# Kernel optimization log

Measured on AMD Instinct MI355X. Metric: run time of the kernel, lower is better.

Reference implementation:

```python
import jax, jax.numpy as jnp
import numpy as np

N_HEADS = 8
TOPK = 32


def setup_inputs() -> dict:
    key = jax.random.key(0)
    ks = jax.random.split(key, 6)
    N, L, Hd = 2, 2048, 512
    s = 1.0 / np.sqrt(Hd).astype(np.float32)
    return {
        "queries": jax.random.normal(ks[0], (N, L, Hd), jnp.float32),
        "keys": jax.random.normal(ks[1], (N, L, Hd), jnp.float32),
        "values": jax.random.normal(ks[2], (N, L, Hd), jnp.float32),
        "Wq": jax.random.normal(ks[3], (Hd, Hd), jnp.float32) * s,
        "bq": jnp.zeros((Hd,), jnp.float32),
        "Wk": jax.random.normal(ks[4], (Hd, Hd), jnp.float32) * s,
        "bk": jnp.zeros((Hd,), jnp.float32),
        "Wv": jax.random.normal(ks[5], (Hd, Hd), jnp.float32) * s,
        "bv": jnp.zeros((Hd,), jnp.float32),
    }


def reference(queries, keys, values, Wq, bq, Wk, bk, Wv, bv):
    N, L, Hd = queries.shape
    S = keys.shape[1]
    H = N_HEADS
    E = Hd // H
    q = (queries @ Wq.T + bq).reshape(N, L, H, E)
    k = (keys @ Wk.T + bk).reshape(N, S, H, E)
    v = (values @ Wv.T + bv).reshape(N, S, H, E)
    temp = 1.0 / np.sqrt(E).astype(np.float32)
    QK = jnp.einsum("nlhe,nshe->nhls", q, k)  # [N,H,L,S]
    topk = min(TOPK, S)
    _, idx = jax.lax.top_k(QK, topk)  # idx: [N,H,L,topk]
    ni = jnp.arange(N)[:, None, None, None]
    hi = jnp.arange(H)[None, :, None, None]
    li = jnp.arange(L)[None, None, :, None]
    keep = jnp.zeros(QK.shape, bool).at[ni, hi, li, idx].set(True)
    # torch: softmax(temp * (QK + mask)) with mask 0 on top-k, -inf elsewhere
    scores = jnp.where(keep, temp * QK, -jnp.inf)
    A = jax.nn.softmax(scores, axis=-1)  # dropout is identity in eval mode
    V = jnp.einsum("nhls,nshd->nlhd", A, v).reshape(N, L, Hd)
    return V, A
```

## Files before the change

kernel.cpp:

```cpp
#include <hip/hip_runtime.h>
#include <cstdint>
#include <cstddef>
#include <math.h>

#define NH     8
#define EH     64
#define HD     512
#define NBATCH 2
#define LSEQ   2048
#define TK     32


using f32x4  = __attribute__((ext_vector_type(4))) float;
using bf16x8 = __attribute__((ext_vector_type(8))) short;

__device__ __forceinline__ unsigned short f2b(float f) {
    unsigned u = __float_as_uint(f);
    return (unsigned short)((u + 0x7FFFu + ((u >> 16) & 1u)) >> 16);
}
__device__ __forceinline__ unsigned f2key(float f) {
    unsigned u = __float_as_uint(f);
    return (u & 0x80000000u) ? ~u : (u | 0x80000000u);
}
__device__ __forceinline__ float key2f(unsigned k) {
    return __uint_as_float((k & 0x80000000u) ? (k ^ 0x80000000u) : ~k);
}

__global__ __launch_bounds__(256) void proj_kernel(
    const float* __restrict__ Xq, const float* __restrict__ Xk, const float* __restrict__ Xv,
    const float* __restrict__ Wq, const float* __restrict__ Bq,
    const float* __restrict__ Wk, const float* __restrict__ Bk,
    const float* __restrict__ Wv, const float* __restrict__ Bv,
    float* __restrict__ ws)
{
    const int z = blockIdx.z;
    const float* X = (z == 0) ? Xq : (z == 1) ? Xk : Xv;
    const float* W = (z == 0) ? Wq : (z == 1) ? Wk : Wv;
    const float* B = (z == 0) ? Bq : (z == 1) ? Bk : Bv;
    float* out = ws + (size_t)z * 2097152;
    unsigned short* khi = (unsigned short*)(ws + 6291456);

    __shared__ float4 Xs[64 * 8];
    __shared__ float4 Ws[64 * 8];

    const int tid = threadIdx.x;
    const int tx = tid & 15, ty = tid >> 4;
    const int m0 = blockIdx.x * 64, n0 = blockIdx.y * 64;

    float acc[4][4];
    #pragma unroll
    for (int i = 0; i < 4; ++i)
        #pragma unroll
        for (int j = 0; j < 4; ++j) acc[i][j] = 0.f;

    for (int k0 = 0; k0 < HD; k0 += 32) {
        #pragma unroll
        for (int it = 0; it < 2; ++it) {
            int f = tid + it * 256;
            int row = f >> 3, c = f & 7;
            int cs = c ^ ((row >> 2) & 7);
            Xs[row * 8 + cs] = *(const float4*)&X[(size_t)(m0 + row) * HD + k0 + c * 4];
            Ws[row * 8 + cs] = *(const float4*)&W[(size_t)(n0 + row) * HD + k0 + c * 4];
        }
        __syncthreads();
        #pragma unroll
        for (int c = 0; c < 8; ++c) {
            float4 av[4], bv4[4];
            #pragma unroll
            for (int i = 0; i < 4; ++i) { int r = ty * 4 + i; av[i]  = Xs[r * 8 + (c ^ ((r >> 2) & 7))]; }
            #pragma unroll
            for (int j = 0; j < 4; ++j) { int r = tx * 4 + j; bv4[j] = Ws[r * 8 + (c ^ ((r >> 2) & 7))]; }
            #pragma unroll
            for (int i = 0; i < 4; ++i)
                #pragma unroll
                for (int j = 0; j < 4; ++j) {
                    acc[i][j] = fmaf(av[i].x, bv4[j].x, acc[i][j]);
                    acc[i][j] = fmaf(av[i].y, bv4[j].y, acc[i][j]);
                    acc[i][j] = fmaf(av[i].z, bv4[j].z, acc[i][j]);
                    acc[i][j] = fmaf(av[i].w, bv4[j].w, acc[i][j]);
                }
        }
        __syncthreads();
    }

    #pragma unroll
    for (int j = 0; j < 4; ++j) {
        int o = n0 + tx * 4 + j;
        float bb = B[o];
        int h = o >> 6, e = o & 63;
        #pragma unroll
        for (int i = 0; i < 4; ++i) {
            int m = m0 + ty * 4 + i;
            int n = m >> 11, s = m & 2047;
            float val = acc[i][j] + bb;
            int head = n * NH + h;
            out[(size_t)head * 131072 + (size_t)s * EH + e] = val;
            if (z == 1) {
                int kt = s >> 4, ks = e >> 5;
                int lane = (((e & 31) >> 3) << 4) | (s & 15);
                size_t idx = ((((size_t)head * 128 + kt) * 2 + ks) * 64 + lane) * 8 + (e & 7);
                khi[idx] = f2b(val);
            }
        }
    }
}

__device__ __forceinline__ unsigned long long sort64_desc(unsigned long long v, int lane) {
    #pragma unroll
    for (int k = 2; k <= 64; k <<= 1)
        #pragma unroll
        for (int j = k >> 1; j >= 1; j >>= 1) {
            unsigned long long o = __shfl_xor(v, j, 64);
            bool up = ((lane & k) != 0);
            bool keepmin = (((lane & j) == 0) == up);
            unsigned long long lo = v < o ? v : o;
            unsigned long long hi = v > o ? v : o;
            v = keepmin ? lo : hi;
        }
    return v;
}
__device__ __forceinline__ unsigned long long merge_top64(unsigned long long a, unsigned long long b, int lane) {
    unsigned long long br = __shfl(b, 63 - lane, 64);
    unsigned long long m = a > br ? a : br;
    #pragma unroll
    for (int j = 32; j >= 1; j >>= 1) {
        unsigned long long o = __shfl_xor(m, j, 64);
        bool keepmax = ((lane & j) == 0);
        unsigned long long mx = m > o ? m : o;
        unsigned long long mn = m < o ? m : o;
        m = keepmax ? mx : mn;
    }
    return m;
}

__global__ __launch_bounds__(512, 4) void attn_kernel(
    const float* __restrict__ ws, float* __restrict__ outV, float* __restrict__ outA)
{
    const float* qw = ws;
    const float* kw = ws + 2097152;
    const float* vw = ws + 4194304;
    const unsigned short* khi = (const unsigned short*)(ws + 6291456);

    __shared__ unsigned short scores16[16 * 2048];
    __shared__ float qs[EH * 16];
    __shared__ unsigned short candArr[8 * 256];
    __shared__ unsigned cnts[8];

    const int tid  = threadIdx.x;
    const int lane = tid & 63;
    const int wv   = tid >> 6;

    unsigned bid = blockIdx.x;
    unsigned id  = (bid & 7u) * 256u + (bid >> 3);
    const int head = (int)(id >> 7);
    const int l0   = (int)(id & 127u) * 16;
    const size_t headoff = (size_t)head * 131072;

    #pragma unroll
    for (int it = 0; it < 2; ++it) {
        int i = tid + it * 512;
        int row = i & 15, e = i >> 4;
        qs[i] = qw[headoff + (size_t)(l0 + row) * EH + e];
    }
    __syncthreads();

    {
        bf16x8 afrag[2];
        #pragma unroll
        for (int ks = 0; ks < 2; ++ks)
            #pragma unroll
            for (int j = 0; j < 8; ++j) {
                int e = ks * 32 + ((lane >> 4) << 3) + j;
                afrag[ks][j] = (short)f2b(qs[e * 16 + (lane & 15)]);
            }

        f32x4 acc[16];
        #pragma unroll
        for (int kt = 0; kt < 16; ++kt) acc[kt] = (f32x4)(0.f);

        const unsigned short* kb = khi + headoff * 2;
        #pragma unroll
        for (int kt = 0; kt < 16; ++kt) {
            int ktg = wv * 16 + kt;
            #pragma unroll
            for (int ks = 0; ks < 2; ++ks) {
                bf16x8 b = *(const bf16x8*)(khi + (size_t)head * 131072 +
                              ((((size_t)ktg * 2 + ks) * 64 + lane) << 3));
                acc[kt] = __builtin_amdgcn_mfma_f32_16x16x32_bf16(afrag[ks], b, acc[kt], 0, 0, 0);
            }
        }
        (void)kb;
        #pragma unroll
        for (int kt = 0; kt < 16; ++kt) {
            int key = wv * 256 + kt * 16 + (lane & 15);
            #pragma unroll
            for (int reg = 0; reg < 4; ++reg) {
                int rr = ((lane >> 4) << 2) + reg;
                scores16[rr * 2048 + key] = (unsigned short)(f2key(acc[kt][reg]) >> 16);
            }
        }
    }
    __syncthreads();

    unsigned short* cand = candArr + wv * 256;
    int   rowS[2][1]; float rowW[2][1];
    int selS[2]; float selW[2];

    #pragma unroll
    for (int rr2 = 0; rr2 < 2; ++rr2) {
        const int r = 2 * wv + rr2;
        const unsigned* srow32 = (const unsigned*)(scores16 + r * 2048);

        unsigned mx = 0;
        #pragma unroll
        for (int t = 0; t < 16; ++t) {
            unsigned vv = srow32[t * 64 + lane];
            unsigned a = vv & 0xFFFFu, b = vv >> 16;
            unsigned ab = a > b ? a : b;
            mx = mx > ab ? mx : ab;
        }
        {
            unsigned v = mx;
            #pragma unroll
            for (int k = 2; k <= 64; k <<= 1)
                #pragma unroll
                for (int j = k >> 1; j >= 1; j >>= 1) {
                    unsigned o = __shfl_xor(v, j);
                    bool up = ((lane & k) == 0);
                    bool keepmin = (((lane & j) == 0) == up);
                    unsigned lo = v < o ? v : o, hi = v > o ? v : o;
                    v = keepmin ? lo : hi;
                }
            mx = __shfl(v, 32);
        }
        const unsigned tau16 = mx;
        const float tauf = key2f(tau16 << 16);
        const unsigned thr16 = f2key(tauf - 0.35f) >> 16;

        if (lane == 0) cnts[wv] = 0;
        #pragma unroll
        for (int t = 0; t < 16; ++t) {
            unsigned vv = srow32[t * 64 + lane];
            unsigned i0 = (unsigned)((t * 64 + lane) * 2);
            if ((vv & 0xFFFFu) >= thr16) {
                unsigned p = atomicAdd(&cnts[wv], 1u);
                if (p < 256) cand[p] = (unsigned short)i0;
            }
            if ((vv >> 16) >= thr16) {
                unsigned p = atomicAdd(&cnts[wv], 1u);
                if (p < 256) cand[p] = (unsigned short)(i0 + 1);
            }
        }
        int Nc = (int)cnts[wv];
        if (Nc > 256) Nc = 256;
        const int nch = (Nc + 63) >> 6;

        unsigned long long best = 0ull;
        for (int c = 0; c < nch; ++c) {
            int p = c * 64 + lane;
            bool valid = p < Nc;
            int si = valid ? (int)cand[p] : 0;
            float sc = 0.f;
            if (valid) {
                const float* krow = kw + headoff + (size_t)si * EH;
                #pragma unroll
                for (int c4 = 0; c4 < 16; ++c4) {
                    float4 kv = *(const float4*)&krow[c4 * 4];
                    sc = fmaf(qs[(c4 * 4 + 0) * 16 + r], kv.x, sc);
                    sc = fmaf(qs[(c4 * 4 + 1) * 16 + r], kv.y, sc);
                    sc = fmaf(qs[(c4 * 4 + 2) * 16 + r], kv.z, sc);
                    sc = fmaf(qs[(c4 * 4 + 3) * 16 + r], kv.w, sc);
                }
            }
            unsigned long long comp = valid
                ? ((((unsigned long long)f2key(sc)) << 32) | (unsigned)(~si))
                : 0ull;
            comp = sort64_desc(comp, lane);
            best = (c == 0) ? comp : merge_top64(best, comp, lane);
        }

        unsigned key32 = (unsigned)(best >> 32);
        int si = (int)(~((unsigned)best)) & 2047;
        float sc = key2f(key32);
        float M = __shfl(sc, 0);
        float ee = (lane < TK) ? __expf(0.125f * (sc - M)) : 0.f;
        float Z = ee;
        #pragma unroll
        for (int d = 1; d < 64; d <<= 1) Z += __shfl_xor(Z, d);
        selS[rr2] = si;
        selW[rr2] = ee / Z;
    }
    rowS[0][0] = selS[0]; rowW[0][0] = selW[0];
    rowS[1][0] = selS[1]; rowW[1][0] = selW[1];

    float* abuf = (float*)((char*)scores16 + wv * 8192);
    const int n = head >> 3, h = head & 7;
    #pragma unroll
    for (int rr2 = 0; rr2 < 2; ++rr2) {
        const int lrow = l0 + 2 * wv + rr2;
        float4* ab4 = (float4*)abuf;
        const float4 z4 = make_float4(0.f, 0.f, 0.f, 0.f);
        #pragma unroll
        for (int u = 0; u < 8; ++u) ab4[u * 64 + lane] = z4;
        if (lane < TK) abuf[rowS[rr2][0]] = rowW[rr2][0];
        float* Arow = outA + ((size_t)head * 2048 + lrow) * 2048;
        #pragma unroll
        for (int u = 0; u < 8; ++u)
            *(float4*)&Arow[(u * 64 + lane) * 4] = ab4[u * 64 + lane];

        float acc = 0.f;
        #pragma unroll
        for (int i = 0; i < TK; ++i) {
            int s_i   = __shfl(rowS[rr2][0], i);
            float w_i = __shfl(rowW[rr2][0], i);
            acc = fmaf(w_i, vw[headoff + (size_t)s_i * EH + lane], acc);
        }
        outV[((size_t)(n * 2048 + lrow)) * 512 + h * 64 + lane] = acc;
    }
}

extern "C" void kernel_launch(void* const* d_in, const int* in_sizes, int n_in,
                              void* d_out, int out_size, void* d_ws, size_t ws_size,
                              hipStream_t stream)
{
    (void)in_sizes; (void)n_in; (void)out_size; (void)ws_size;
    const float* q  = (const float*)d_in[0];
    const float* k  = (const float*)d_in[1];
    const float* v  = (const float*)d_in[2];
    const float* Wq = (const float*)d_in[3];
    const float* bq = (const float*)d_in[4];
    const float* Wk = (const float*)d_in[5];
    const float* bk = (const float*)d_in[6];
    const float* Wv = (const float*)d_in[7];
    const float* bv = (const float*)d_in[8];
    float* ws   = (float*)d_ws;
    float* outV = (float*)d_out;
    float* outA = outV + (size_t)NBATCH * LSEQ * HD;

    proj_kernel<<<dim3(64, 8, 3), 256, 0, stream>>>(q, k, v, Wq, bq, Wk, bk, Wv, bv, ws);
    attn_kernel<<<dim3(2048, 1, 1), 512, 0, stream>>>(ws, outV, outA);
}
```

Before: 246.2 us.

## Coalesce bf16 key staging and replace atomics/shuffles with ballots and readlanes

The projection kernel now stages bf16 keys in shared memory and writes the MFMA-ready layout with 16-byte vector stores instead of scattered 2-byte stores. In the attention kernel, the LDS atomic candidate compaction becomes ballot/popcount prefix compaction. Row scores are held in registers instead of re-read from LDS, and q rows are loaded into registers for exact rescoring. Per-tile MFMA accumulators are shortened in lifetime, and shuffles in the V gather become readlane. These changes raise register use and add LDS usage in the projection kernel.

```diff
diff --git a/kernel.cpp b/kernel.cpp
--- a/kernel.cpp
+++ b/kernel.cpp
@@ -13,6 +13,7 @@
 
 using f32x4  = __attribute__((ext_vector_type(4))) float;
 using bf16x8 = __attribute__((ext_vector_type(8))) short;
+using u16x8  = __attribute__((ext_vector_type(8))) unsigned short;
 
 __device__ __forceinline__ unsigned short f2b(float f) {
     unsigned u = __float_as_uint(f);
@@ -25,6 +26,7 @@
 __device__ __forceinline__ float key2f(unsigned k) {
     return __uint_as_float((k & 0x80000000u) ? (k ^ 0x80000000u) : ~k);
 }
+__device__ __forceinline__ unsigned umax2(unsigned a, unsigned b) { return a > b ? a : b; }
 
 __global__ __launch_bounds__(256) void proj_kernel(
     const float* __restrict__ Xq, const float* __restrict__ Xk, const float* __restrict__ Xv,
@@ -42,6 +44,7 @@
 
     __shared__ float4 Xs[64 * 8];
     __shared__ float4 Ws[64 * 8];
+    __shared__ unsigned short kst[64 * 72];
 
     const int tid = threadIdx.x;
     const int tx = tid & 15, ty = tid >> 4;
@@ -95,12 +98,25 @@
             float val = acc[i][j] + bb;
             int head = n * NH + h;
             out[(size_t)head * 131072 + (size_t)s * EH + e] = val;
-            if (z == 1) {
-                int kt = s >> 4, ks = e >> 5;
-                int lane = (((e & 31) >> 3) << 4) | (s & 15);
-                size_t idx = ((((size_t)head * 128 + kt) * 2 + ks) * 64 + lane) * 8 + (e & 7);
-                khi[idx] = f2b(val);
-            }
+            if (z == 1) kst[(ty * 4 + i) * 72 + e] = f2b(val);
+        }
+    }
+
+    if (z == 1) {
+        __syncthreads();
+        const int head = (m0 >> 11) * NH + (n0 >> 6);
+        const int kt0  = (m0 & 2047) >> 4;
+        #pragma unroll
+        for (int it = 0; it < 2; ++it) {
+            int g = tid + it * 256;
+            int lane_g = g & 63;
+            int rest = g >> 6;
+            int kt = rest >> 1, ksb = rest & 1;
+            int s_loc = kt * 16 + (lane_g & 15);
+            int e0 = ksb * 32 + ((lane_g >> 4) << 3);
+            u16x8 vv = *(const u16x8*)&kst[s_loc * 72 + e0];
+            size_t idx = ((((size_t)head * 128 + (kt0 + kt)) * 2 + ksb) * 64 + lane_g) * 8;
+            *(u16x8*)&khi[idx] = vv;
         }
     }
 }
@@ -144,11 +160,10 @@
     __shared__ unsigned short scores16[16 * 2048];
     __shared__ float qs[EH * 16];
     __shared__ unsigned short candArr[8 * 256];
-    __shared__ unsigned cnts[8];
 
     const int tid  = threadIdx.x;
     const int lane = tid & 63;
-    const int wv   = tid >> 6;
+    const int uwv  = __builtin_amdgcn_readfirstlane(tid) >> 6;
 
     unsigned bid = blockIdx.x;
     unsigned id  = (bid & 7u) * 256u + (bid >> 3);
@@ -174,50 +189,44 @@
                 afrag[ks][j] = (short)f2b(qs[e * 16 + (lane & 15)]);
             }
 
-        f32x4 acc[16];
-        #pragma unroll
-        for (int kt = 0; kt < 16; ++kt) acc[kt] = (f32x4)(0.f);
-
-        const unsigned short* kb = khi + headoff * 2;
         #pragma unroll
         for (int kt = 0; kt < 16; ++kt) {
-            int ktg = wv * 16 + kt;
+            f32x4 acc = (f32x4)(0.f);
+            int ktg = uwv * 16 + kt;
             #pragma unroll
             for (int ks = 0; ks < 2; ++ks) {
                 bf16x8 b = *(const bf16x8*)(khi + (size_t)head * 131072 +
                               ((((size_t)ktg * 2 + ks) * 64 + lane) << 3));
-                acc[kt] = __builtin_amdgcn_mfma_f32_16x16x32_bf16(afrag[ks], b, acc[kt], 0, 0, 0);
-            }
-        }
-        (void)kb;
-        #pragma unroll
-        for (int kt = 0; kt < 16; ++kt) {
-            int key = wv * 256 + kt * 16 + (lane & 15);
-            #pragma unroll
-            for (int reg = 0; reg < 4; ++reg) {
-                int rr = ((lane >> 4) << 2) + reg;
-                scores16[rr * 2048 + key] = (unsigned short)(f2key(acc[kt][reg]) >> 16);
-            }
+                acc = __builtin_amdgcn_mfma_f32_16x16x32_bf16(afrag[ks], b, acc, 0, 0, 0);
+            }
+            int key = uwv * 256 + kt * 16 + (lane & 15);
+            int rbase = (lane >> 4) << 2;
+            #pragma unroll
+            for (int reg = 0; reg < 4; ++reg)
+                scores16[(rbase + reg) * 2048 + key] = (unsigned short)(f2key(acc[reg]) >> 16);
         }
     }
     __syncthreads();
 
-    unsigned short* cand = candArr + wv * 256;
-    int   rowS[2][1]; float rowW[2][1];
+    unsigned short* cand = candArr + uwv * 256;
+    const unsigned long long lmlt = (1ull << lane) - 1ull;
     int selS[2]; float selW[2];
 
     #pragma unroll
     for (int rr2 = 0; rr2 < 2; ++rr2) {
-        const int r = 2 * wv + rr2;
+        const int r = 2 * uwv + rr2;
+        const int lrow = l0 + r;
         const unsigned* srow32 = (const unsigned*)(scores16 + r * 2048);
 
+        unsigned pk[16];
+        #pragma unroll
+        for (int t = 0; t < 16; ++t) pk[t] = srow32[t * 64 + lane];
+
         unsigned mx = 0;
         #pragma unroll
         for (int t = 0; t < 16; ++t) {
-            unsigned vv = srow32[t * 64 + lane];
-            unsigned a = vv & 0xFFFFu, b = vv >> 16;
-            unsigned ab = a > b ? a : b;
-            mx = mx > ab ? mx : ab;
+            unsigned a = pk[t] & 0xFFFFu, b = pk[t] >> 16;
+            mx = umax2(mx, umax2(a, b));
         }
         {
             unsigned v = mx;
@@ -237,40 +246,48 @@
         const float tauf = key2f(tau16 << 16);
         const unsigned thr16 = f2key(tauf - 0.35f) >> 16;
 
-        if (lane == 0) cnts[wv] = 0;
+        int Nc = 0;
         #pragma unroll
         for (int t = 0; t < 16; ++t) {
-            unsigned vv = srow32[t * 64 + lane];
+            unsigned vv = pk[t];
             unsigned i0 = (unsigned)((t * 64 + lane) * 2);
-            if ((vv & 0xFFFFu) >= thr16) {
-                unsigned p = atomicAdd(&cnts[wv], 1u);
+            bool c0 = (vv & 0xFFFFu) >= thr16;
+            bool c1 = (vv >> 16) >= thr16;
+            unsigned long long b0 = __ballot(c0);
+            if (c0) {
+                int p = Nc + __popcll(b0 & lmlt);
                 if (p < 256) cand[p] = (unsigned short)i0;
             }
-            if ((vv >> 16) >= thr16) {
-                unsigned p = atomicAdd(&cnts[wv], 1u);
+            Nc += __popcll(b0);
+            unsigned long long b1 = __ballot(c1);
+            if (c1) {
+                int p = Nc + __popcll(b1 & lmlt);
                 if (p < 256) cand[p] = (unsigned short)(i0 + 1);
             }
-        }
-        int Nc = (int)cnts[wv];
+            Nc += __popcll(b1);
+        }
         if (Nc > 256) Nc = 256;
         const int nch = (Nc + 63) >> 6;
+
+        const float* qrow = qw + headoff + (size_t)lrow * EH;
+        float4 qv[16];
+        #pragma unroll
+        for (int c4 = 0; c4 < 16; ++c4) qv[c4] = *(const float4*)&qrow[c4 * 4];
 
         unsigned long long best = 0ull;
         for (int c = 0; c < nch; ++c) {
             int p = c * 64 + lane;
             bool valid = p < Nc;
             int si = valid ? (int)cand[p] : 0;
+            const float* krow = kw + headoff + (size_t)si * EH;
             float sc = 0.f;
-            if (valid) {
-                const float* krow = kw + headoff + (size_t)si * EH;
-                #pragma unroll
-                for (int c4 = 0; c4 < 16; ++c4) {
-                    float4 kv = *(const float4*)&krow[c4 * 4];
-                    sc = fmaf(qs[(c4 * 4 + 0) * 16 + r], kv.x, sc);
-                    sc = fmaf(qs[(c4 * 4 + 1) * 16 + r], kv.y, sc);
-                    sc = fmaf(qs[(c4 * 4 + 2) * 16 + r], kv.z, sc);
-                    sc = fmaf(qs[(c4 * 4 + 3) * 16 + r], kv.w, sc);
-                }
+            #pragma unroll
+            for (int c4 = 0; c4 < 16; ++c4) {
+                float4 kv = *(const float4*)&krow[c4 * 4];
+                sc = fmaf(qv[c4].x, kv.x, sc);
+                sc = fmaf(qv[c4].y, kv.y, sc);
+                sc = fmaf(qv[c4].z, kv.z, sc);
+                sc = fmaf(qv[c4].w, kv.w, sc);
             }
             unsigned long long comp = valid
                 ? ((((unsigned long long)f2key(sc)) << 32) | (unsigned)(~si))
@@ -290,31 +307,31 @@
         selS[rr2] = si;
         selW[rr2] = ee / Z;
     }
-    rowS[0][0] = selS[0]; rowW[0][0] = selW[0];
-    rowS[1][0] = selS[1]; rowW[1][0] = selW[1];
-
-    float* abuf = (float*)((char*)scores16 + wv * 8192);
-    const int n = head >> 3, h = head & 7;
+
+    float* abuf = (float*)((char*)scores16 + uwv * 8192);
     #pragma unroll
     for (int rr2 = 0; rr2 < 2; ++rr2) {
-        const int lrow = l0 + 2 * wv + rr2;
+        const int lrow = l0 + 2 * uwv + rr2;
         float4* ab4 = (float4*)abuf;
         const float4 z4 = make_float4(0.f, 0.f, 0.f, 0.f);
         #pragma unroll
         for (int u = 0; u < 8; ++u) ab4[u * 64 + lane] = z4;
-        if (lane < TK) abuf[rowS[rr2][0]] = rowW[rr2][0];
+        if (lane < TK) abuf[selS[rr2]] = selW[rr2];
         float* Arow = outA + ((size_t)head * 2048 + lrow) * 2048;
         #pragma unroll
         for (int u = 0; u < 8; ++u)
             *(float4*)&Arow[(u * 64 + lane) * 4] = ab4[u * 64 + lane];
 
         float acc = 0.f;
+        int   siv = selS[rr2];
+        unsigned wbits = __float_as_uint(selW[rr2]);
         #pragma unroll
         for (int i = 0; i < TK; ++i) {
-            int s_i   = __shfl(rowS[rr2][0], i);
-            float w_i = __shfl(rowW[rr2][0], i);
+            int s_i   = __builtin_amdgcn_readlane(siv, i);
+            float w_i = __uint_as_float((unsigned)__builtin_amdgcn_readlane((int)wbits, i));
             acc = fmaf(w_i, vw[headoff + (size_t)s_i * EH + lane], acc);
         }
+        const int n = head >> 3, h = head & 7;
         outV[((size_t)(n * 2048 + lrow)) * 512 + h * 64 + lane] = acc;
     }
 }
```

After: 221.6 us. 10.0% less time.
